# Performance work log

Measured on AMD Instinct MI355X. Metric: run time of the kernel, lower is better.

Reference implementation:

```python
import jax, jax.numpy as jnp
import numpy as np

B = 8192

def setup_inputs() -> dict:
    key = jax.random.key(0)
    k1, k2, k3 = jax.random.split(key, 3)
    risk_pred = jax.random.normal(k1, (B, 1), dtype=jnp.float32)
    time = jax.random.uniform(k2, (B,), dtype=jnp.float32)
    event = jax.random.randint(k3, (B,), 0, 2, dtype=jnp.int32)
    return {"risk_pred": risk_pred, "time": time, "event": event}

def reference(risk_pred, time, event):
    # Faithful vectorization of the O(B^2) double loop over ordered pairs i<j.
    r = jnp.squeeze(risk_pred)
    n = r.shape[0]
    upper = jnp.triu(jnp.ones((n, n), dtype=bool), k=1)  # i < j pairs only
    ti, tj = time[:, None], time[None, :]
    ri, rj = r[:, None], r[None, :]
    ei = (event == 1)[:, None]
    ej_cens = (event == 0)[None, :]
    ej_ev = (event == 1)[None, :]

    # Case A: event_i==1, event_j==0, time_i < time_j
    maskA = upper & ei & ej_cens & (ti < tj)
    # Case B: event_i==1, event_j==1
    maskB = upper & ei & ej_ev

    concA = maskA & (ri > rj)
    concB = maskB & (((ti < tj) & (ri > rj)) | ((ti > tj) & (ri < rj)))
    tiedM = (maskA | maskB) & (ri == rj)

    f32 = jnp.float32
    concordant = jnp.sum(concA.astype(f32)) + jnp.sum(concB.astype(f32))
    tied = 0.5 * jnp.sum(tiedM.astype(f32))
    comparable = jnp.sum(maskA.astype(f32)) + jnp.sum(maskB.astype(f32))

    c_index = jnp.where(comparable > 0,
                        (concordant + tied) / jnp.maximum(comparable, 1.0),
                        jnp.float32(0.5))
    return 1.0 - c_index
```

## Files before the change

kernel.cpp:

```cpp
#include <hip/hip_runtime.h>

#define TILE 256

__global__ __launch_bounds__(256) void cindex_pairs_kernel(
    const float* __restrict__ risk,
    const float* __restrict__ tim,
    const int*   __restrict__ evt,
    unsigned int* __restrict__ part,
    int n, int nblk)
{
    const int t = blockIdx.x;
    int p = (int)((sqrtf(8.0f * (float)t + 1.0f) - 1.0f) * 0.5f);
    while ((p + 1) * (p + 2) / 2 <= t) ++p;
    while (p * (p + 1) / 2 > t) --p;
    const int q = t - p * (p + 1) / 2;

    const int i0 = q * TILE;
    const int j0 = p * TILE;
    const bool diag = (p == q);

    __shared__ float2 s_pack[TILE];
    __shared__ int    s_idx[TILE];
    __shared__ unsigned int s_cnt[4];
    __shared__ unsigned int s_part[4][3];

    const int tid  = threadIdx.x;
    const int wid  = tid >> 6;
    const int lane = tid & 63;

    {
        int i = i0 + tid;
        bool inb = (i < n);
        float tv = inb ? tim[i]  : 0.0f;
        float rv = inb ? risk[i] : 0.0f;
        bool ev = inb && (evt[i] == 1);
        unsigned long long m = __ballot(ev);
        if (lane == 0) s_cnt[wid] = (unsigned int)__popcll(m);
        __syncthreads();
        int base = 0;
        #pragma unroll
        for (int w = 0; w < 4; ++w) base += (w < wid) ? (int)s_cnt[w] : 0;
        int pos = base + (int)__popcll(m & ((1ull << lane) - 1ull));
        if (ev) { s_pack[pos] = make_float2(tv, rv); s_idx[pos] = tid; }
    }
    __syncthreads();

    int cnt = (int)(s_cnt[0] + s_cnt[1] + s_cnt[2] + s_cnt[3]);
    cnt = __builtin_amdgcn_readfirstlane(cnt);

    const int j  = j0 + tid;
    const bool jv = (j < n);
    const float tj = jv ? tim[j]  : 0.0f;
    const float rj = jv ? risk[j] : 0.0f;
    const int  ejv = jv ? evt[j]  : -1;
    const bool ej1 = (ejv == 1);
    const bool ej0 = (ejv == 0);

    unsigned int nComp = 0, nConc = 0, nTie = 0;

    if (!diag) {
        #pragma unroll 4
        for (int k = 0; k < cnt; ++k) {
            float2 tr = s_pack[k];
            float ti = tr.x, ri = tr.y;
            bool lt  = ti < tj;
            bool gt  = ti > tj;
            bool rgt = ri > rj;
            bool rlt = ri < rj;
            bool req = ri == rj;
            bool comp = ej1 | (ej0 & lt);
            bool conc = (ej1 & ((lt & rgt) | (gt & rlt))) | (ej0 & lt & rgt);
            nComp += (unsigned int)comp;
            nConc += (unsigned int)conc;
            nTie  += (unsigned int)(comp & req);
        }
    } else {
        #pragma unroll 4
        for (int k = 0; k < cnt; ++k) {
            float2 tr = s_pack[k];
            int   ii  = s_idx[k];
            float ti = tr.x, ri = tr.y;
            bool ok  = tid > ii;
            bool lt  = ti < tj;
            bool gt  = ti > tj;
            bool rgt = ri > rj;
            bool rlt = ri < rj;
            bool req = ri == rj;
            bool comp = (ej1 | (ej0 & lt)) & ok;
            bool conc = ((ej1 & ((lt & rgt) | (gt & rlt))) | (ej0 & lt & rgt)) & ok;
            nComp += (unsigned int)comp;
            nConc += (unsigned int)conc;
            nTie  += (unsigned int)(comp & req);
        }
    }

    for (int off = 32; off > 0; off >>= 1) {
        nComp += __shfl_down(nComp, off, 64);
        nConc += __shfl_down(nConc, off, 64);
        nTie  += __shfl_down(nTie,  off, 64);
    }
    if (lane == 0) {
        s_part[wid][0] = nConc;
        s_part[wid][1] = nTie;
        s_part[wid][2] = nComp;
    }
    __syncthreads();
    if (tid == 0) {
        unsigned int c0 = 0, c1 = 0, c2 = 0;
        #pragma unroll
        for (int w = 0; w < 4; ++w) {
            c0 += s_part[w][0];
            c1 += s_part[w][1];
            c2 += s_part[w][2];
        }
        part[t] = c0;
        part[nblk + t] = c1;
        part[2 * nblk + t] = c2;
    }
}

__global__ __launch_bounds__(256) void cindex_reduce_kernel(
    const unsigned int* __restrict__ part,
    float* __restrict__ out, int nblk)
{
    const int tid = threadIdx.x;
    unsigned int c0 = 0, c1 = 0, c2 = 0;
    for (int i = tid; i < nblk; i += 256) {
        c0 += part[i];
        c1 += part[nblk + i];
        c2 += part[2 * nblk + i];
    }
    for (int off = 32; off > 0; off >>= 1) {
        c0 += __shfl_down(c0, off, 64);
        c1 += __shfl_down(c1, off, 64);
        c2 += __shfl_down(c2, off, 64);
    }
    __shared__ unsigned int s_part[4][3];
    const int wid  = tid >> 6;
    const int lane = tid & 63;
    if (lane == 0) {
        s_part[wid][0] = c0;
        s_part[wid][1] = c1;
        s_part[wid][2] = c2;
    }
    __syncthreads();
    if (tid == 0) {
        unsigned int t0 = 0, t1 = 0, t2 = 0;
        #pragma unroll
        for (int w = 0; w < 4; ++w) {
            t0 += s_part[w][0];
            t1 += s_part[w][1];
            t2 += s_part[w][2];
        }
        double conc = (double)t0;
        double tie  = (double)t1;
        double comp = (double)t2;
        float c;
        if (comp > 0.0) {
            c = (float)((conc + 0.5 * tie) / comp);
        } else {
            c = 0.5f;
        }
        out[0] = 1.0f - c;
    }
}

extern "C" void kernel_launch(void* const* d_in, const int* in_sizes, int n_in,
                              void* d_out, int out_size, void* d_ws, size_t ws_size,
                              hipStream_t stream)
{
    const float* risk = (const float*)d_in[0];
    const float* tim  = (const float*)d_in[1];
    const int*   evt  = (const int*)d_in[2];
    float* out = (float*)d_out;
    unsigned int* part = (unsigned int*)d_ws;

    const int n = in_sizes[1];
    const int nt = (n + TILE - 1) / TILE;
    const int nblk = nt * (nt + 1) / 2;

    cindex_pairs_kernel<<<dim3(nblk), 256, 0, stream>>>(risk, tim, evt, part, n, nblk);
    cindex_reduce_kernel<<<1, 256, 0, stream>>>(part, out, nblk);
}
```

Before: 20.79 us.

## Fuse the final reduction into the pairs kernel using per-block ready flags

```diff
diff --git a/kernel.cpp b/kernel.cpp
--- a/kernel.cpp
+++ b/kernel.cpp
@@ -1,12 +1,15 @@
 #include <hip/hip_runtime.h>
 
 #define TILE 256
+#define MAGIC 0x5AFEC0DEu
 
-__global__ __launch_bounds__(256) void cindex_pairs_kernel(
+__global__ __launch_bounds__(256) void cindex_onepass_kernel(
     const float* __restrict__ risk,
     const float* __restrict__ tim,
     const int*   __restrict__ evt,
     unsigned int* __restrict__ part,
+    unsigned int* __restrict__ flags,
+    float* __restrict__ out,
     int n, int nblk)
 {
     const int t = blockIdx.x;
@@ -116,52 +119,57 @@
         part[t] = c0;
         part[nblk + t] = c1;
         part[2 * nblk + t] = c2;
+        __hip_atomic_store(&flags[t], MAGIC ^ (unsigned int)t,
+                           __ATOMIC_RELEASE, __HIP_MEMORY_SCOPE_AGENT);
     }
-}
 
-__global__ __launch_bounds__(256) void cindex_reduce_kernel(
-    const unsigned int* __restrict__ part,
-    float* __restrict__ out, int nblk)
-{
-    const int tid = threadIdx.x;
-    unsigned int c0 = 0, c1 = 0, c2 = 0;
-    for (int i = tid; i < nblk; i += 256) {
-        c0 += part[i];
-        c1 += part[nblk + i];
-        c2 += part[2 * nblk + i];
-    }
-    for (int off = 32; off > 0; off >>= 1) {
-        c0 += __shfl_down(c0, off, 64);
-        c1 += __shfl_down(c1, off, 64);
-        c2 += __shfl_down(c2, off, 64);
-    }
-    __shared__ unsigned int s_part[4][3];
-    const int wid  = tid >> 6;
-    const int lane = tid & 63;
-    if (lane == 0) {
-        s_part[wid][0] = c0;
-        s_part[wid][1] = c1;
-        s_part[wid][2] = c2;
-    }
-    __syncthreads();
-    if (tid == 0) {
-        unsigned int t0 = 0, t1 = 0, t2 = 0;
-        #pragma unroll
-        for (int w = 0; w < 4; ++w) {
-            t0 += s_part[w][0];
-            t1 += s_part[w][1];
-            t2 += s_part[w][2];
+    if (t == 0) {
+        for (int i = tid; i < nblk; i += 256) {
+            while (__hip_atomic_load(&flags[i], __ATOMIC_ACQUIRE,
+                                     __HIP_MEMORY_SCOPE_AGENT)
+                   != (MAGIC ^ (unsigned int)i)) {
+                __builtin_amdgcn_s_sleep(1);
+            }
         }
-        double conc = (double)t0;
-        double tie  = (double)t1;
-        double comp = (double)t2;
-        float c;
-        if (comp > 0.0) {
-            c = (float)((conc + 0.5 * tie) / comp);
-        } else {
-            c = 0.5f;
+        __syncthreads();
+
+        unsigned int c0 = 0, c1 = 0, c2 = 0;
+        for (int i = tid; i < nblk; i += 256) {
+            c0 += __hip_atomic_load(&part[i],            __ATOMIC_RELAXED, __HIP_MEMORY_SCOPE_AGENT);
+            c1 += __hip_atomic_load(&part[nblk + i],     __ATOMIC_RELAXED, __HIP_MEMORY_SCOPE_AGENT);
+            c2 += __hip_atomic_load(&part[2 * nblk + i], __ATOMIC_RELAXED, __HIP_MEMORY_SCOPE_AGENT);
         }
-        out[0] = 1.0f - c;
+        for (int off = 32; off > 0; off >>= 1) {
+            c0 += __shfl_down(c0, off, 64);
+            c1 += __shfl_down(c1, off, 64);
+            c2 += __shfl_down(c2, off, 64);
+        }
+        __syncthreads();
+        if (lane == 0) {
+            s_part[wid][0] = c0;
+            s_part[wid][1] = c1;
+            s_part[wid][2] = c2;
+        }
+        __syncthreads();
+        if (tid == 0) {
+            unsigned int t0 = 0, t1 = 0, t2 = 0;
+            #pragma unroll
+            for (int w = 0; w < 4; ++w) {
+                t0 += s_part[w][0];
+                t1 += s_part[w][1];
+                t2 += s_part[w][2];
+            }
+            double conc = (double)t0;
+            double tie  = (double)t1;
+            double comp = (double)t2;
+            float c;
+            if (comp > 0.0) {
+                c = (float)((conc + 0.5 * tie) / comp);
+            } else {
+                c = 0.5f;
+            }
+            out[0] = 1.0f - c;
+        }
     }
 }
 
@@ -173,12 +181,13 @@
     const float* tim  = (const float*)d_in[1];
     const int*   evt  = (const int*)d_in[2];
     float* out = (float*)d_out;
-    unsigned int* part = (unsigned int*)d_ws;
+    unsigned int* part  = (unsigned int*)d_ws;
 
     const int n = in_sizes[1];
     const int nt = (n + TILE - 1) / TILE;
     const int nblk = nt * (nt + 1) / 2;
+    unsigned int* flags = part + 3 * nblk;
 
-    cindex_pairs_kernel<<<dim3(nblk), 256, 0, stream>>>(risk, tim, evt, part, n, nblk);
-    cindex_reduce_kernel<<<1, 256, 0, stream>>>(part, out, nblk);
+    cindex_onepass_kernel<<<dim3(nblk), 256, 0, stream>>>(
+        risk, tim, evt, part, flags, out, n, nblk);
 }
```

Result: slower. 23.11 us (+11.2%).

## Sort j-tile lanes by event status to specialize inner loops without divergence

Applied to the files above, without the earlier changes.

```diff
diff --git a/kernel.cpp b/kernel.cpp
--- a/kernel.cpp
+++ b/kernel.cpp
@@ -19,9 +19,11 @@
     const int j0 = p * TILE;
     const bool diag = (p == q);
 
-    __shared__ float2 s_pack[TILE];
-    __shared__ int    s_idx[TILE];
-    __shared__ unsigned int s_cnt[4];
+    __shared__ float2 s_ipack[TILE];
+    __shared__ int    s_iidx[TILE];
+    __shared__ float2 s_jpack[TILE];
+    __shared__ int    s_jorig[TILE];
+    __shared__ unsigned int s_icnt[4], s_ecnt[4], s_ccnt[4];
     __shared__ unsigned int s_part[4][3];
 
     const int tid  = threadIdx.x;
@@ -30,67 +32,137 @@
 
     {
         int i = i0 + tid;
-        bool inb = (i < n);
-        float tv = inb ? tim[i]  : 0.0f;
-        float rv = inb ? risk[i] : 0.0f;
-        bool ev = inb && (evt[i] == 1);
-        unsigned long long m = __ballot(ev);
-        if (lane == 0) s_cnt[wid] = (unsigned int)__popcll(m);
+        bool ivalid = (i < n);
+        float tv = ivalid ? tim[i]  : 0.0f;
+        float rv = ivalid ? risk[i] : 0.0f;
+        bool iev = ivalid && (evt[i] == 1);
+
+        int j = j0 + tid;
+        bool jvalid = (j < n);
+        float tjv = jvalid ? tim[j]  : 0.0f;
+        float rjv = jvalid ? risk[j] : 0.0f;
+        int  e    = jvalid ? evt[j]  : -1;
+        bool jev = (e == 1);
+        bool jce = (e == 0);
+
+        unsigned long long mi = __ballot(iev);
+        unsigned long long me = __ballot(jev);
+        unsigned long long mc = __ballot(jce);
+        if (lane == 0) {
+            s_icnt[wid] = (unsigned int)__popcll(mi);
+            s_ecnt[wid] = (unsigned int)__popcll(me);
+            s_ccnt[wid] = (unsigned int)__popcll(mc);
+        }
         __syncthreads();
-        int base = 0;
+
+        int ib = 0, eb = 0, cb = 0, ncT = 0, neT = 0;
         #pragma unroll
-        for (int w = 0; w < 4; ++w) base += (w < wid) ? (int)s_cnt[w] : 0;
-        int pos = base + (int)__popcll(m & ((1ull << lane) - 1ull));
-        if (ev) { s_pack[pos] = make_float2(tv, rv); s_idx[pos] = tid; }
-    }
-    __syncthreads();
-
-    int cnt = (int)(s_cnt[0] + s_cnt[1] + s_cnt[2] + s_cnt[3]);
+        for (int w = 0; w < 4; ++w) {
+            if (w < wid) { ib += (int)s_icnt[w]; eb += (int)s_ecnt[w]; cb += (int)s_ccnt[w]; }
+            ncT += (int)s_ccnt[w];
+            neT += (int)s_ecnt[w];
+        }
+        unsigned long long below = (1ull << lane) - 1ull;
+        if (iev) {
+            int pos = ib + (int)__popcll(mi & below);
+            s_ipack[pos] = make_float2(tv, rv);
+            s_iidx[pos]  = tid;
+        }
+        if (jev) {
+            int pos = ncT + eb + (int)__popcll(me & below);
+            s_jpack[pos] = make_float2(tjv, rjv);
+            s_jorig[pos] = tid;
+        }
+        if (jce) {
+            int pos = cb + (int)__popcll(mc & below);
+            s_jpack[pos] = make_float2(tjv, rjv);
+            s_jorig[pos] = tid;
+        }
+        if (tid >= ncT + neT) {
+            float nanf_ = __uint_as_float(0x7fc00000u);
+            s_jpack[tid] = make_float2(nanf_, nanf_);
+            s_jorig[tid] = -1;
+        }
+        __syncthreads();
+    }
+
+    int cnt = (int)(s_icnt[0] + s_icnt[1] + s_icnt[2] + s_icnt[3]);
     cnt = __builtin_amdgcn_readfirstlane(cnt);
-
-    const int j  = j0 + tid;
-    const bool jv = (j < n);
-    const float tj = jv ? tim[j]  : 0.0f;
-    const float rj = jv ? risk[j] : 0.0f;
-    const int  ejv = jv ? evt[j]  : -1;
-    const bool ej1 = (ejv == 1);
-    const bool ej0 = (ejv == 0);
+    int nc  = (int)(s_ccnt[0] + s_ccnt[1] + s_ccnt[2] + s_ccnt[3]);
+    nc  = __builtin_amdgcn_readfirstlane(nc);
+    int ne  = (int)(s_ecnt[0] + s_ecnt[1] + s_ecnt[2] + s_ecnt[3]);
+    ne  = __builtin_amdgcn_readfirstlane(ne);
+
+    float2 jp = s_jpack[tid];
+    const float tj = jp.x;
+    const float rj = jp.y;
+    const int jorig = s_jorig[tid];
+    const bool laneEv = (tid >= nc) && (tid < nc + ne);
 
     unsigned int nComp = 0, nConc = 0, nTie = 0;
 
     if (!diag) {
-        #pragma unroll 4
-        for (int k = 0; k < cnt; ++k) {
-            float2 tr = s_pack[k];
-            float ti = tr.x, ri = tr.y;
-            bool lt  = ti < tj;
-            bool gt  = ti > tj;
-            bool rgt = ri > rj;
-            bool rlt = ri < rj;
-            bool req = ri == rj;
-            bool comp = ej1 | (ej0 & lt);
-            bool conc = (ej1 & ((lt & rgt) | (gt & rlt))) | (ej0 & lt & rgt);
-            nComp += (unsigned int)comp;
-            nConc += (unsigned int)conc;
-            nTie  += (unsigned int)(comp & req);
+        if (laneEv) {
+            nComp = (unsigned int)cnt;
+            #pragma unroll 4
+            for (int k = 0; k < cnt; ++k) {
+                float2 tr = s_ipack[k];
+                float ti = tr.x, ri = tr.y;
+                bool lt  = ti < tj;
+                bool gt  = ti > tj;
+                bool rgt = ri > rj;
+                bool rlt = ri < rj;
+                bool req = ri == rj;
+                bool conc = (lt & rgt) | (gt & rlt);
+                nConc += (unsigned int)conc;
+                nTie  += (unsigned int)req;
+            }
+        } else {
+            #pragma unroll 4
+            for (int k = 0; k < cnt; ++k) {
+                float2 tr = s_ipack[k];
+                float ti = tr.x, ri = tr.y;
+                bool lt  = ti < tj;
+                bool rgt = ri > rj;
+                bool req = ri == rj;
+                nComp += (unsigned int)lt;
+                nConc += (unsigned int)(lt & rgt);
+                nTie  += (unsigned int)(lt & req);
+            }
         }
     } else {
-        #pragma unroll 4
-        for (int k = 0; k < cnt; ++k) {
-            float2 tr = s_pack[k];
-            int   ii  = s_idx[k];
-            float ti = tr.x, ri = tr.y;
-            bool ok  = tid > ii;
-            bool lt  = ti < tj;
-            bool gt  = ti > tj;
-            bool rgt = ri > rj;
-            bool rlt = ri < rj;
-            bool req = ri == rj;
-            bool comp = (ej1 | (ej0 & lt)) & ok;
-            bool conc = ((ej1 & ((lt & rgt) | (gt & rlt))) | (ej0 & lt & rgt)) & ok;
-            nComp += (unsigned int)comp;
-            nConc += (unsigned int)conc;
-            nTie  += (unsigned int)(comp & req);
+        if (laneEv) {
+            #pragma unroll 4
+            for (int k = 0; k < cnt; ++k) {
+                float2 tr = s_ipack[k];
+                int   ii  = s_iidx[k];
+                float ti = tr.x, ri = tr.y;
+                bool ok  = jorig > ii;
+                bool lt  = ti < tj;
+                bool gt  = ti > tj;
+                bool rgt = ri > rj;
+                bool rlt = ri < rj;
+                bool req = ri == rj;
+                bool conc = (lt & rgt) | (gt & rlt);
+                nComp += (unsigned int)ok;
+                nConc += (unsigned int)(ok & conc);
+                nTie  += (unsigned int)(ok & req);
+            }
+        } else {
+            #pragma unroll 4
+            for (int k = 0; k < cnt; ++k) {
+                float2 tr = s_ipack[k];
+                int   ii  = s_iidx[k];
+                float ti = tr.x, ri = tr.y;
+                bool ok  = jorig > ii;
+                bool lt  = ti < tj;
+                bool rgt = ri > rj;
+                bool req = ri == rj;
+                bool c   = ok & lt;
+                nComp += (unsigned int)c;
+                nConc += (unsigned int)(c & rgt);
+                nTie  += (unsigned int)(c & req);
+            }
         }
     }
 
```

Result: slower. 21.36 us (+2.7%).

## Use single-wavefront 64-wide tiles and drop cross-wave shared reductions

Applied to the files above, without the earlier changes.

```diff
diff --git a/kernel.cpp b/kernel.cpp
--- a/kernel.cpp
+++ b/kernel.cpp
@@ -1,8 +1,8 @@
 #include <hip/hip_runtime.h>
 
-#define TILE 256
+#define TILE 64
 
-__global__ __launch_bounds__(256) void cindex_pairs_kernel(
+__global__ __launch_bounds__(64) void cindex_pairs_kernel(
     const float* __restrict__ risk,
     const float* __restrict__ tim,
     const int*   __restrict__ evt,
@@ -21,13 +21,10 @@
 
     __shared__ float2 s_pack[TILE];
     __shared__ int    s_idx[TILE];
-    __shared__ unsigned int s_cnt[4];
-    __shared__ unsigned int s_part[4][3];
 
-    const int tid  = threadIdx.x;
-    const int wid  = tid >> 6;
-    const int lane = tid & 63;
+    const int tid = threadIdx.x;
 
+    int cnt;
     {
         int i = i0 + tid;
         bool inb = (i < n);
@@ -35,17 +32,11 @@
         float rv = inb ? risk[i] : 0.0f;
         bool ev = inb && (evt[i] == 1);
         unsigned long long m = __ballot(ev);
-        if (lane == 0) s_cnt[wid] = (unsigned int)__popcll(m);
-        __syncthreads();
-        int base = 0;
-        #pragma unroll
-        for (int w = 0; w < 4; ++w) base += (w < wid) ? (int)s_cnt[w] : 0;
-        int pos = base + (int)__popcll(m & ((1ull << lane) - 1ull));
+        cnt = (int)__popcll(m);
+        int pos = (int)__popcll(m & ((1ull << tid) - 1ull));
         if (ev) { s_pack[pos] = make_float2(tv, rv); s_idx[pos] = tid; }
     }
     __syncthreads();
-
-    int cnt = (int)(s_cnt[0] + s_cnt[1] + s_cnt[2] + s_cnt[3]);
     cnt = __builtin_amdgcn_readfirstlane(cnt);
 
     const int j  = j0 + tid;
@@ -99,33 +90,20 @@
         nConc += __shfl_down(nConc, off, 64);
         nTie  += __shfl_down(nTie,  off, 64);
     }
-    if (lane == 0) {
-        s_part[wid][0] = nConc;
-        s_part[wid][1] = nTie;
-        s_part[wid][2] = nComp;
-    }
-    __syncthreads();
     if (tid == 0) {
-        unsigned int c0 = 0, c1 = 0, c2 = 0;
-        #pragma unroll
-        for (int w = 0; w < 4; ++w) {
-            c0 += s_part[w][0];
-            c1 += s_part[w][1];
-            c2 += s_part[w][2];
-        }
-        part[t] = c0;
-        part[nblk + t] = c1;
-        part[2 * nblk + t] = c2;
+        part[t] = nConc;
+        part[nblk + t] = nTie;
+        part[2 * nblk + t] = nComp;
     }
 }
 
-__global__ __launch_bounds__(256) void cindex_reduce_kernel(
+__global__ __launch_bounds__(1024) void cindex_reduce_kernel(
     const unsigned int* __restrict__ part,
     float* __restrict__ out, int nblk)
 {
     const int tid = threadIdx.x;
     unsigned int c0 = 0, c1 = 0, c2 = 0;
-    for (int i = tid; i < nblk; i += 256) {
+    for (int i = tid; i < nblk; i += 1024) {
         c0 += part[i];
         c1 += part[nblk + i];
         c2 += part[2 * nblk + i];
@@ -135,7 +113,7 @@
         c1 += __shfl_down(c1, off, 64);
         c2 += __shfl_down(c2, off, 64);
     }
-    __shared__ unsigned int s_part[4][3];
+    __shared__ unsigned int s_part[16][3];
     const int wid  = tid >> 6;
     const int lane = tid & 63;
     if (lane == 0) {
@@ -147,7 +125,7 @@
     if (tid == 0) {
         unsigned int t0 = 0, t1 = 0, t2 = 0;
         #pragma unroll
-        for (int w = 0; w < 4; ++w) {
+        for (int w = 0; w < 16; ++w) {
             t0 += s_part[w][0];
             t1 += s_part[w][1];
             t2 += s_part[w][2];
@@ -179,6 +157,6 @@
     const int nt = (n + TILE - 1) / TILE;
     const int nblk = nt * (nt + 1) / 2;
 
-    cindex_pairs_kernel<<<dim3(nblk), 256, 0, stream>>>(risk, tim, evt, part, n, nblk);
-    cindex_reduce_kernel<<<1, 256, 0, stream>>>(part, out, nblk);
+    cindex_pairs_kernel<<<dim3(nblk), TILE, 0, stream>>>(risk, tim, evt, part, n, nblk);
+    cindex_reduce_kernel<<<1, 1024, 0, stream>>>(part, out, nblk);
 }
```

After: 18.47 us. -11.2%, faster.
